# Optimization experiments

Hardware: AMD Instinct MI355X
Metric: run time of the kernel (lower is better)

The kernel has to match this reference:

```python
import jax, jax.numpy as jnp
import numpy as np

B, R, H, F = 65536, 64, 10, 5


def setup_inputs() -> dict:
    key = jax.random.key(0)
    ks = jax.random.split(key, 14)
    return {
        "r_emb": jax.random.normal(ks[0], (B, R, H), jnp.float32),
        "feature": jax.random.normal(ks[1], (B, F), jnp.float32),
        "h0": jax.random.normal(ks[2], (B, H), jnp.float32),
        "c0": jax.random.normal(ks[3], (B, H), jnp.float32),
        "W_ih": jax.random.normal(ks[4], (4 * H, H), jnp.float32) * 0.3,
        "W_hh": jax.random.normal(ks[5], (4 * H, H), jnp.float32) * 0.3,
        "b_ih": jax.random.normal(ks[6], (4 * H,), jnp.float32) * 0.1,
        "b_hh": jax.random.normal(ks[7], (4 * H,), jnp.float32) * 0.1,
        "Wr": jax.random.normal(ks[8], (H, H), jnp.float32) * 0.3,
        "br": jax.random.normal(ks[9], (H,), jnp.float32) * 0.1,
        "Wh": jax.random.normal(ks[10], (H, H), jnp.float32) * 0.3,
        "bh": jax.random.normal(ks[11], (H,), jnp.float32) * 0.1,
        "Wfc": jax.random.normal(ks[12], (1, R * H + F), jnp.float32) * 0.1,
        "bfc": jax.random.normal(ks[13], (1,), jnp.float32) * 0.1,
    }


def reference(r_emb, feature, h0, c0, W_ih, W_hh, b_ih, b_hh, Wr, br, Wh, bh, Wfc, bfc):
    # r_emb: [B, R, H] -> scan over regions (time-major [R, B, H])
    xs = jnp.swapaxes(r_emb, 0, 1)

    def step(carry, x_t):
        h, c = carry
        # PyTorch LSTMCell gate order: i, f, g, o
        gates = x_t @ W_ih.T + b_ih + h @ W_hh.T + b_hh  # [B, 4H]
        i, f, g, o = jnp.split(gates, 4, axis=-1)
        c_new = jax.nn.sigmoid(f) * c + jax.nn.sigmoid(i) * jnp.tanh(g)
        h_new = jax.nn.sigmoid(o) * jnp.tanh(c_new)
        gate = jax.nn.sigmoid(x_t @ Wr.T + br + h_new @ Wh.T + bh)
        return (h_new, c_new), h_new * gate

    (_, _), outs = jax.lax.scan(step, (h0, c0), xs)  # outs: [R, B, H]
    flat = jnp.swapaxes(outs, 0, 1).reshape(r_emb.shape[0], -1)  # [B, R*H]
    fc_in = jnp.concatenate([flat, feature], axis=1)  # [B, R*H + F]
    return fc_in @ Wfc.T + bfc  # [B, 1]
```

## Files before the change

kernel.cpp:

```cpp
#include <hip/hip_runtime.h>

#define Rn 64
#define Hn 10
#define Fn 5

__device__ __forceinline__ float fsigmoid(float x) {
    return __builtin_amdgcn_rcpf(1.0f + __expf(-x));
}
__device__ __forceinline__ float ftanh(float x) {
    return 1.0f - 2.0f * __builtin_amdgcn_rcpf(__expf(2.0f * x) + 1.0f);
}

__global__ __launch_bounds__(256, 2) void seqreader_kernel(
    const float* __restrict__ r_emb,
    const float* __restrict__ feature,
    const float* __restrict__ h0,
    const float* __restrict__ c0,
    const float* __restrict__ W_ih,
    const float* __restrict__ W_hh,
    const float* __restrict__ b_ih,
    const float* __restrict__ b_hh,
    const float* __restrict__ Wr,
    const float* __restrict__ br,
    const float* __restrict__ Wh,
    const float* __restrict__ bh,
    const float* __restrict__ Wfc,
    const float* __restrict__ bfc,
    float* __restrict__ out)
{
    __shared__ __align__(16) float sWih[40 * 12];
    __shared__ __align__(16) float sWhh[40 * 12];
    __shared__ __align__(16) float sWr[10 * 12];
    __shared__ __align__(16) float sWhn[10 * 12];
    __shared__ float sWfc[646];
    __shared__ float sX[2][128 * 41];

    const int tid  = threadIdx.x;
    const int lane = tid & 63;
    const int half = lane >> 5;
    const int r0h  = half * 5;
    const int bb   = (tid >> 6) * 32 + (lane & 31);
    const int b0   = blockIdx.x * 128;
    const int b    = b0 + bb;

    for (int i = tid; i < 400; i += 256) {
        int r = i / 10, k = i - r * 10;
        sWih[r * 12 + k] = W_ih[i];
        sWhh[r * 12 + k] = W_hh[i];
    }
    for (int i = tid; i < 100; i += 256) {
        int r = i / 10, k = i - r * 10;
        sWr[r * 12 + k]  = Wr[i];
        sWhn[r * 12 + k] = Wh[i];
    }
    for (int i = tid; i < 645; i += 256) sWfc[i] = Wfc[i];

    float bi[5], bf_[5], bg_[5], bo[5], brh[5];
#pragma unroll
    for (int j = 0; j < 5; ++j) {
        bi[j]  = b_ih[0  + r0h + j] + b_hh[0  + r0h + j];
        bf_[j] = b_ih[10 + r0h + j] + b_hh[10 + r0h + j];
        bg_[j] = b_ih[20 + r0h + j] + b_hh[20 + r0h + j];
        bo[j]  = b_ih[30 + r0h + j] + b_hh[30 + r0h + j];
        brh[j] = br[r0h + j] + bh[r0h + j];
    }

    float c[5];
#pragma unroll
    for (int j = 0; j < 5; ++j) c[j] = c0[b * Hn + r0h + j];
    float hf[Hn];
#pragma unroll
    for (int k = 0; k < Hn; ++k) hf[k] = h0[b * Hn + k];

    float acc = 0.0f;
    if (half == 0) {
        acc = bfc[0];
#pragma unroll
        for (int k = 0; k < Fn; ++k)
            acc = fmaf(feature[b * Fn + k], Wfc[Rn * Hn + k], acc);
    }

    unsigned off_g[5], off_l[5];
#pragma unroll
    for (int k = 0; k < 5; ++k) {
        int q  = k * 256 + tid;
        int bq = q / 10;
        int e  = q - bq * 10;
        off_g[k] = (unsigned)((bq * (Rn * Hn) + e * 4) * 4);
        off_l[k] = (unsigned)(bq * 41 + e * 4);
    }
    const char* gb = (const char*)(r_emb + (size_t)b0 * (Rn * Hn));

    {
        float4 s0[5];
#pragma unroll
        for (int k = 0; k < 5; ++k) s0[k] = *(const float4*)(gb + off_g[k]);
#pragma unroll
        for (int k = 0; k < 5; ++k) {
            float* d = &sX[0][off_l[k]];
            d[0] = s0[k].x; d[1] = s0[k].y; d[2] = s0[k].z; d[3] = s0[k].w;
        }
    }
    __syncthreads();

    float4 st[5];
#pragma unroll 1
    for (int t = 0; t < Rn; ++t) {
        const int tt = t & 3;
        const int Tb = (t >> 2) & 1;

        if (tt == 0 && t + 4 < Rn) {
#pragma unroll
            for (int k = 0; k < 5; ++k)
                st[k] = *(const float4*)(gb + off_g[k] + (unsigned)(t / 4 + 1) * 160u);
        }

        float x[Hn];
        const float* xr = &sX[Tb][bb * 41 + tt * Hn];
#pragma unroll
        for (int j = 0; j < Hn; ++j) x[j] = xr[j];

        float hn[5];
#pragma unroll
        for (int j = 0; j < 5; ++j) {
            float si = bi[j], sf = bf_[j], sg = bg_[j], so = bo[j];
#pragma unroll
            for (int k = 0; k < Hn; ++k) {
                const float xk = x[k], hk = hf[k];
                si = fmaf(sWih[(0  + r0h + j) * 12 + k], xk, si);
                si = fmaf(sWhh[(0  + r0h + j) * 12 + k], hk, si);
                sf = fmaf(sWih[(10 + r0h + j) * 12 + k], xk, sf);
                sf = fmaf(sWhh[(10 + r0h + j) * 12 + k], hk, sf);
                sg = fmaf(sWih[(20 + r0h + j) * 12 + k], xk, sg);
                sg = fmaf(sWhh[(20 + r0h + j) * 12 + k], hk, sg);
                so = fmaf(sWih[(30 + r0h + j) * 12 + k], xk, so);
                so = fmaf(sWhh[(30 + r0h + j) * 12 + k], hk, so);
            }
            const float cn = fsigmoid(sf) * c[j] + fsigmoid(si) * ftanh(sg);
            c[j] = cn;
            hn[j] = fsigmoid(so) * ftanh(cn);
        }

        float sw[5];
#pragma unroll
        for (int j = 0; j < 5; ++j) sw[j] = __shfl_xor(hn[j], 32, 64);
#pragma unroll
        for (int j = 0; j < 5; ++j) {
            hf[j]     = half ? sw[j] : hn[j];
            hf[5 + j] = half ? hn[j] : sw[j];
        }

        if (tt == 2 && t + 2 < Rn) {
#pragma unroll
            for (int k = 0; k < 5; ++k) {
                float* d = &sX[Tb ^ 1][off_l[k]];
                d[0] = st[k].x; d[1] = st[k].y; d[2] = st[k].z; d[3] = st[k].w;
            }
        }

#pragma unroll
        for (int j = 0; j < 5; ++j) {
            float s = brh[j];
#pragma unroll
            for (int k = 0; k < Hn; ++k) {
                s = fmaf(sWr[(r0h + j) * 12 + k], x[k], s);
                s = fmaf(sWhn[(r0h + j) * 12 + k], hf[k], s);
            }
            acc = fmaf(hn[j] * fsigmoid(s), sWfc[t * Hn + r0h + j], acc);
        }

        if (tt == 3) __syncthreads();
    }

    acc += __shfl_xor(acc, 32, 64);
    if (half == 0) out[b] = acc;
}

extern "C" void kernel_launch(void* const* d_in, const int* in_sizes, int n_in,
                              void* d_out, int out_size, void* d_ws, size_t ws_size,
                              hipStream_t stream) {
    const float* r_emb   = (const float*)d_in[0];
    const float* feature = (const float*)d_in[1];
    const float* h0      = (const float*)d_in[2];
    const float* c0      = (const float*)d_in[3];
    const float* W_ih    = (const float*)d_in[4];
    const float* W_hh    = (const float*)d_in[5];
    const float* b_ih    = (const float*)d_in[6];
    const float* b_hh    = (const float*)d_in[7];
    const float* Wr      = (const float*)d_in[8];
    const float* br      = (const float*)d_in[9];
    const float* Wh      = (const float*)d_in[10];
    const float* bh      = (const float*)d_in[11];
    const float* Wfc     = (const float*)d_in[12];
    const float* bfc     = (const float*)d_in[13];
    float* out = (float*)d_out;

    dim3 grid(65536 / 128), block(256);
    hipLaunchKernelGGL(seqreader_kernel, grid, block, 0, stream,
                       r_emb, feature, h0, c0, W_ih, W_hh, b_ih, b_hh,
                       Wr, br, Wh, bh, Wfc, bfc, out);
}
```

Measured before the change: 210.8 us.

## Use packed FP32 FMA and 16-byte-aligned LDS rows for LSTM gate dot products

Each LSTM gate and output-gate dot product is rewritten as a 2-wide vector FMA chain (v_pk_fma_f32). The inner loops now load weights and x as float4 from LDS instead of scalar reads. The LDS staging of r_emb is relaid out to a 52-float row stride, with each timestep padded to 12 floats so x can be read as aligned float4. This should roughly halve the FMA instruction count and cut LDS read instructions. In exchange, the staging stores become scattered scalar writes with extra offset registers, and the summation order changes slightly.

```diff
diff --git a/kernel.cpp b/kernel.cpp
--- a/kernel.cpp
+++ b/kernel.cpp
@@ -3,6 +3,12 @@
 #define Rn 64
 #define Hn 10
 #define Fn 5
+#define XRS 52
+
+typedef float f32x2 __attribute__((ext_vector_type(2)));
+typedef float f32x4 __attribute__((ext_vector_type(4)));
+
+#define PKFMA(a, b, c) __builtin_elementwise_fma((a), (b), (c))
 
 __device__ __forceinline__ float fsigmoid(float x) {
     return __builtin_amdgcn_rcpf(1.0f + __expf(-x));
@@ -33,7 +39,7 @@
     __shared__ __align__(16) float sWr[10 * 12];
     __shared__ __align__(16) float sWhn[10 * 12];
     __shared__ float sWfc[646];
-    __shared__ float sX[2][128 * 41];
+    __shared__ __align__(16) float sX[2][128 * XRS];
 
     const int tid  = threadIdx.x;
     const int lane = tid & 63;
@@ -80,14 +86,19 @@
             acc = fmaf(feature[b * Fn + k], Wfc[Rn * Hn + k], acc);
     }
 
-    unsigned off_g[5], off_l[5];
+    unsigned off_g[5], off_l[5][4];
 #pragma unroll
     for (int k = 0; k < 5; ++k) {
         int q  = k * 256 + tid;
         int bq = q / 10;
         int e  = q - bq * 10;
         off_g[k] = (unsigned)((bq * (Rn * Hn) + e * 4) * 4);
-        off_l[k] = (unsigned)(bq * 41 + e * 4);
+#pragma unroll
+        for (int cidx = 0; cidx < 4; ++cidx) {
+            int u = e * 4 + cidx;
+            int s = u / 10, kk = u - s * 10;
+            off_l[k][cidx] = (unsigned)(bq * XRS + s * 12 + kk);
+        }
     }
     const char* gb = (const char*)(r_emb + (size_t)b0 * (Rn * Hn));
 
@@ -97,8 +108,10 @@
         for (int k = 0; k < 5; ++k) s0[k] = *(const float4*)(gb + off_g[k]);
 #pragma unroll
         for (int k = 0; k < 5; ++k) {
-            float* d = &sX[0][off_l[k]];
-            d[0] = s0[k].x; d[1] = s0[k].y; d[2] = s0[k].z; d[3] = s0[k].w;
+            sX[0][off_l[k][0]] = s0[k].x;
+            sX[0][off_l[k][1]] = s0[k].y;
+            sX[0][off_l[k][2]] = s0[k].z;
+            sX[0][off_l[k][3]] = s0[k].w;
         }
     }
     __syncthreads();
@@ -115,30 +128,45 @@
                 st[k] = *(const float4*)(gb + off_g[k] + (unsigned)(t / 4 + 1) * 160u);
         }
 
-        float x[Hn];
-        const float* xr = &sX[Tb][bb * 41 + tt * Hn];
-#pragma unroll
-        for (int j = 0; j < Hn; ++j) x[j] = xr[j];
+        const f32x4* xr = (const f32x4*)&sX[Tb][bb * XRS + tt * 12];
+        const f32x4 xq0 = xr[0], xq1 = xr[1], xq2 = xr[2];
+        const f32x2 x01 = xq0.lo, x23 = xq0.hi, x45 = xq1.lo, x67 = xq1.hi, x89 = xq2.lo;
+
+        f32x2 h2[5];
+#pragma unroll
+        for (int p = 0; p < 5; ++p) h2[p] = f32x2{hf[2 * p], hf[2 * p + 1]};
 
         float hn[5];
 #pragma unroll
         for (int j = 0; j < 5; ++j) {
-            float si = bi[j], sf = bf_[j], sg = bg_[j], so = bo[j];
-#pragma unroll
-            for (int k = 0; k < Hn; ++k) {
-                const float xk = x[k], hk = hf[k];
-                si = fmaf(sWih[(0  + r0h + j) * 12 + k], xk, si);
-                si = fmaf(sWhh[(0  + r0h + j) * 12 + k], hk, si);
-                sf = fmaf(sWih[(10 + r0h + j) * 12 + k], xk, sf);
-                sf = fmaf(sWhh[(10 + r0h + j) * 12 + k], hk, sf);
-                sg = fmaf(sWih[(20 + r0h + j) * 12 + k], xk, sg);
-                sg = fmaf(sWhh[(20 + r0h + j) * 12 + k], hk, sg);
-                so = fmaf(sWih[(30 + r0h + j) * 12 + k], xk, so);
-                so = fmaf(sWhh[(30 + r0h + j) * 12 + k], hk, so);
+            float zg[4];
+#pragma unroll
+            for (int gidx = 0; gidx < 4; ++gidx) {
+                const int row = gidx * 10 + r0h + j;
+                const f32x4* wi = (const f32x4*)&sWih[row * 12];
+                const f32x4* wh = (const f32x4*)&sWhh[row * 12];
+                const f32x4 wi0 = wi[0], wi1 = wi[1], wi2 = wi[2];
+                const f32x4 wh0 = wh[0], wh1 = wh[1], wh2 = wh[2];
+                f32x2 z2 = {0.f, 0.f};
+                z2 = PKFMA(wi0.lo, x01, z2);
+                z2 = PKFMA(wi0.hi, x23, z2);
+                z2 = PKFMA(wi1.lo, x45, z2);
+                z2 = PKFMA(wi1.hi, x67, z2);
+                z2 = PKFMA(wi2.lo, x89, z2);
+                z2 = PKFMA(wh0.lo, h2[0], z2);
+                z2 = PKFMA(wh0.hi, h2[1], z2);
+                z2 = PKFMA(wh1.lo, h2[2], z2);
+                z2 = PKFMA(wh1.hi, h2[3], z2);
+                z2 = PKFMA(wh2.lo, h2[4], z2);
+                zg[gidx] = z2[0] + z2[1];
             }
-            const float cn = fsigmoid(sf) * c[j] + fsigmoid(si) * ftanh(sg);
+            const float si = fsigmoid(zg[0] + bi[j]);
+            const float sf = fsigmoid(zg[1] + bf_[j]);
+            const float tg = ftanh(zg[2] + bg_[j]);
+            const float so = fsigmoid(zg[3] + bo[j]);
+            const float cn = fmaf(sf, c[j], si * tg);
             c[j] = cn;
-            hn[j] = fsigmoid(so) * ftanh(cn);
+            hn[j] = so * ftanh(cn);
         }
 
         float sw[5];
@@ -153,19 +181,35 @@
         if (tt == 2 && t + 2 < Rn) {
 #pragma unroll
             for (int k = 0; k < 5; ++k) {
-                float* d = &sX[Tb ^ 1][off_l[k]];
-                d[0] = st[k].x; d[1] = st[k].y; d[2] = st[k].z; d[3] = st[k].w;
+                sX[Tb ^ 1][off_l[k][0]] = st[k].x;
+                sX[Tb ^ 1][off_l[k][1]] = st[k].y;
+                sX[Tb ^ 1][off_l[k][2]] = st[k].z;
+                sX[Tb ^ 1][off_l[k][3]] = st[k].w;
             }
         }
 
+        f32x2 hn2[5];
+#pragma unroll
+        for (int p = 0; p < 5; ++p) hn2[p] = f32x2{hf[2 * p], hf[2 * p + 1]};
 #pragma unroll
         for (int j = 0; j < 5; ++j) {
-            float s = brh[j];
-#pragma unroll
-            for (int k = 0; k < Hn; ++k) {
-                s = fmaf(sWr[(r0h + j) * 12 + k], x[k], s);
-                s = fmaf(sWhn[(r0h + j) * 12 + k], hf[k], s);
-            }
+            const int row = r0h + j;
+            const f32x4* wr_ = (const f32x4*)&sWr[row * 12];
+            const f32x4* wh_ = (const f32x4*)&sWhn[row * 12];
+            const f32x4 wr0 = wr_[0], wr1 = wr_[1], wr2 = wr_[2];
+            const f32x4 wh0 = wh_[0], wh1 = wh_[1], wh2 = wh_[2];
+            f32x2 z2 = {0.f, 0.f};
+            z2 = PKFMA(wr0.lo, x01, z2);
+            z2 = PKFMA(wr0.hi, x23, z2);
+            z2 = PKFMA(wr1.lo, x45, z2);
+            z2 = PKFMA(wr1.hi, x67, z2);
+            z2 = PKFMA(wr2.lo, x89, z2);
+            z2 = PKFMA(wh0.lo, hn2[0], z2);
+            z2 = PKFMA(wh0.hi, hn2[1], z2);
+            z2 = PKFMA(wh1.lo, hn2[2], z2);
+            z2 = PKFMA(wh1.hi, hn2[3], z2);
+            z2 = PKFMA(wh2.lo, hn2[4], z2);
+            const float s = z2[0] + z2[1] + brh[j];
             acc = fmaf(hn[j] * fsigmoid(s), sWfc[t * Hn + r0h + j], acc);
         }
 
```

New measurement: 211.5 us. About the same (+0.4%).
